# Kernel tuning notes

Hardware: AMD Instinct MI355X
Metric: run time of the kernel (lower is better)

## Reference

```python
import jax, jax.numpy as jnp
import numpy as np

B, S, H = 2, 2048, 1024
NH, HD = 16, 64
EPS = 1e-12
SCALE = float(np.sqrt(HD))


def layer_norm(x, g, b, eps=EPS):
    m = jnp.mean(x, axis=-1, keepdims=True)
    v = jnp.mean(jnp.square(x - m), axis=-1, keepdims=True)
    return (x - m) * jax.lax.rsqrt(v + eps) * g + b


def setup_inputs() -> dict:
    key = jax.random.key(0)
    ks = jax.random.split(key, 12)
    std = 0.02 / np.sqrt(2 * 24)  # num_hidden_layers = 24
    return {
        "hidden_states": jax.random.normal(ks[0], (B, S, H), dtype=jnp.float32),
        "attention_mask": jnp.ones((B, S), dtype=jnp.float32),
        "Wq": jax.random.normal(ks[1], (H, H), dtype=jnp.float32) * std,
        "bq": jnp.zeros((H,), dtype=jnp.float32),
        "Wk": jax.random.normal(ks[2], (H, H), dtype=jnp.float32) * std,
        "bk": jnp.zeros((H,), dtype=jnp.float32),
        "Wv": jax.random.normal(ks[3], (H, H), dtype=jnp.float32) * std,
        "bv": jnp.zeros((H,), dtype=jnp.float32),
        "Wd": jax.random.normal(ks[4], (H, H), dtype=jnp.float32) * (1.0 / np.sqrt(H)),
        "bd": jnp.zeros((H,), dtype=jnp.float32),
        "ln_g": jnp.ones((H,), dtype=jnp.float32),
        "ln_b": jnp.zeros((H,), dtype=jnp.float32),
    }


def reference(hidden_states, attention_mask, Wq, bq, Wk, bk, Wv, bv, Wd, bd, ln_g, ln_b):
    x = hidden_states
    # NOTE: source computes pre_attention_norm(x) but the no-cache path uses raw x for Q/K/V.
    def heads(t):  # [B,S,H] -> [B,NH,S,HD]
        return t.reshape(B, S, NH, HD).transpose(0, 2, 1, 3)

    q = heads(x @ Wq.T + bq)
    k = heads(x @ Wk.T + bk)
    v = heads(x @ Wv.T + bv)

    scores = jnp.einsum("bhqd,bhkd->bhqk", q, k) / SCALE
    mask = (1.0 - attention_mask) * -10000.0  # [B,S] -> broadcast [B,1,1,S]
    scores = scores + mask[:, None, None, :]
    probs = jax.nn.softmax(scores.astype(jnp.float32), axis=-1).astype(x.dtype)

    ctx = jnp.einsum("bhqk,bhkd->bhqd", probs, v)
    ctx = ctx.transpose(0, 2, 1, 3).reshape(B, S, NH * HD)

    out = ctx @ Wd.T + bd
    out = layer_norm(out + x, ln_g, ln_b)
    out = jnp.where(jnp.isfinite(out), out, jnp.zeros_like(out))
    return out
```

## Files before the change

### kernel.cpp

```cpp
#include <hip/hip_runtime.h>
#include <cstdint>
#include <cstddef>

#define B_    2
#define S_    2048
#define H_    1024
#define NH_   16
#define HD_   64

typedef __attribute__((ext_vector_type(8))) __bf16 bf16x8;
typedef __attribute__((ext_vector_type(4))) __bf16 bf16x4;
typedef __attribute__((ext_vector_type(4))) float  f32x4;
typedef __attribute__((ext_vector_type(2))) unsigned u32x2;

typedef __attribute__((address_space(1))) const unsigned int gcu32_t;
typedef __attribute__((address_space(3))) unsigned int lu32_t;
#define GLOAD16(gp, lp) __builtin_amdgcn_global_load_lds((gcu32_t*)(gp), (lu32_t*)(lp), 16, 0, 0)

#if __has_builtin(__builtin_amdgcn_exp2f)
#define EXP2F(x) __builtin_amdgcn_exp2f(x)
#else
#define EXP2F(x) exp2f(x)
#endif

#define SC_Q 0.1803368977f

__device__ __forceinline__ short f2bf(float f) {
  union { float f; unsigned u; } v; v.f = f;
  unsigned r = v.u + 0x7fffu + ((v.u >> 16) & 1u);
  return (short)(r >> 16);
}

__global__ __launch_bounds__(256) void convert_kernel(
    const float* __restrict__ x,  const float* __restrict__ wq,
    const float* __restrict__ wk, const float* __restrict__ wv,
    const float* __restrict__ wd,
    short* __restrict__ xb,  short* __restrict__ wqb, short* __restrict__ wkb,
    short* __restrict__ wvb, short* __restrict__ wdb) {
  size_t i = ((size_t)blockIdx.x * 256 + threadIdx.x) * 4;
  const float* src; short* dst; size_t off;
  if      (i < 4194304u) { src = x;  dst = xb;  off = i; }
  else if (i < 5242880u) { src = wq; dst = wqb; off = i - 4194304u; }
  else if (i < 6291456u) { src = wk; dst = wkb; off = i - 5242880u; }
  else if (i < 7340032u) { src = wv; dst = wvb; off = i - 6291456u; }
  else                   { src = wd; dst = wdb; off = i - 7340032u; }
  float4 v = *(const float4*)(src + off);
  short4 o; o.x = f2bf(v.x); o.y = f2bf(v.y); o.z = f2bf(v.z); o.w = f2bf(v.w);
  *(short4*)(dst + off) = o;
}

template<int MODE>
__global__ __launch_bounds__(256, 3) void gemm_bt(
    const short* __restrict__ A,
    const short* __restrict__ Bq, const short* __restrict__ Bk,
    const short* __restrict__ Bv,
    const float* __restrict__ biasq, const float* __restrict__ biask,
    const float* __restrict__ biasv,
    short* __restrict__ outq, short* __restrict__ outk, short* __restrict__ outv,
    float* __restrict__ outy) {
  __shared__ short As[128 * 64];
  __shared__ short Bs[128 * 64];

  const short* Bw; const float* bias; short* outs = nullptr;
  float qscale = 1.0f;
  if (MODE == 0) {
    int z = blockIdx.z;
    Bw   = (z == 0) ? Bq    : ((z == 1) ? Bk    : Bv);
    bias = (z == 0) ? biasq : ((z == 1) ? biask : biasv);
    outs = (z == 0) ? outq  : ((z == 1) ? outk  : outv);
    if (z == 0) qscale = SC_Q;
  } else {
    Bw = Bq; bias = biasq;
  }

  const int K = 1024;
  int tid  = threadIdx.x;
  int lane = tid & 63, w = tid >> 6;
  int wr = w >> 1, wc = w & 1;
  int m0 = blockIdx.y * 128, n0 = blockIdx.x * 128;
  int l15 = lane & 15, lg = lane >> 4;

  int lr = lane >> 3, lc8 = 8 * ((lane & 7) ^ lr);
  const short* Ag = A  + (size_t)(m0 + w * 8 + lr) * K + lc8;
  const short* Bg = Bw + (size_t)(n0 + w * 8 + lr) * K + lc8;

  int cxor = (l15 & 7) * 8;

  f32x4 acc[4][4];
  for (int m = 0; m < 4; m++)
    for (int n = 0; n < 4; n++) acc[m][n] = {0.f, 0.f, 0.f, 0.f};

  for (int kt = 0; kt < 16; kt++) {
    __syncthreads();
    for (int it = 0; it < 4; it++) {
      GLOAD16(Ag + (size_t)it * 32 * K + kt * 64, &As[(w * 8 + it * 32) * 64]);
      GLOAD16(Bg + (size_t)it * 32 * K + kt * 64, &Bs[(w * 8 + it * 32) * 64]);
    }
    __syncthreads();
    __builtin_amdgcn_s_setprio(1);
#pragma unroll
    for (int kkh = 0; kkh < 2; kkh++) {
      int col = (kkh * 32 + lg * 8) ^ cxor;
      bf16x8 af[4], bfr[4];
#pragma unroll
      for (int m = 0; m < 4; m++)
        af[m] = *(const bf16x8*)&As[(wr * 64 + m * 16 + l15) * 64 + col];
#pragma unroll
      for (int n = 0; n < 4; n++)
        bfr[n] = *(const bf16x8*)&Bs[(wc * 64 + n * 16 + l15) * 64 + col];
#pragma unroll
      for (int m = 0; m < 4; m++)
#pragma unroll
        for (int n = 0; n < 4; n++)
          acc[m][n] = __builtin_amdgcn_mfma_f32_16x16x32_bf16(af[m], bfr[n], acc[m][n], 0, 0, 0);
    }
    __builtin_amdgcn_s_setprio(0);
  }

  for (int n = 0; n < 4; n++) {
    int col = n0 + wc * 64 + n * 16 + l15;
    float bval = bias[col];
    if (MODE == 0) {
      int h = col >> 6, d = col & 63;
      for (int m = 0; m < 4; m++) {
        int rowb = m0 + wr * 64 + m * 16 + lg * 4;
        for (int j = 0; j < 4; j++) {
          int row = rowb + j;
          int bb = row >> 11, s = row & 2047;
          outs[(((size_t)bb * NH_ + h) * S_ + s) * HD_ + d] = f2bf((acc[m][n][j] + bval) * qscale);
        }
      }
    } else {
      for (int m = 0; m < 4; m++) {
        int rowb = m0 + wr * 64 + m * 16 + lg * 4;
        for (int j = 0; j < 4; j++)
          outy[(size_t)(rowb + j) * 1024 + col] = acc[m][n][j] + bval;
      }
    }
  }
}

__global__ __launch_bounds__(256, 2) void attn_kernel(
    const short* __restrict__ Q, const short* __restrict__ K,
    const short* __restrict__ V, const float* __restrict__ mask,
    short* __restrict__ ctx) {
  __shared__ short QPs[128 * 72];
  __shared__ short Ks[2][64 * 64];
  __shared__ short Vs[2][64 * 64];
  __shared__ float msk[2][64];

  int b = blockIdx.x;
  int bh = (b & 7) * 4 + ((b >> 3) >> 4);
  int qb = (b >> 3) & 15;
  int bidx = bh >> 4, h = bh & 15;
  int q0 = qb * 128;
  int tid = threadIdx.x, lane = tid & 63, w = tid >> 6;
  int l15 = lane & 15, lg = lane >> 4;

  const short* Qg = Q + (size_t)bh * S_ * HD_;
  const short* Kg = K + (size_t)bh * S_ * HD_;
  const short* Vg = V + (size_t)bh * S_ * HD_;

  int lr = lane >> 3, lc8 = 8 * ((lane & 7) ^ lr);
  int cxor = (l15 & 7) * 8;
  const float MLOG2E = -10000.0f * 1.442695041f;

  for (int it = 0; it < 4; it++) {
    int r = w * 8 + it * 32;
    GLOAD16(Qg + (size_t)(q0 + r + lr) * HD_ + lc8, &QPs[r * 64]);
  }
  for (int it = 0; it < 2; it++) {
    int r = w * 8 + it * 32;
    GLOAD16(Kg + (size_t)(r + lr) * HD_ + lc8, &Ks[0][r * 64]);
  }
  int vrow = tid >> 3, vcol = (tid & 7) * 8;
  int voff = ((vrow >> 2) * 4 + (vcol >> 4)) * 64 + (vrow & 3) * 16 + (vcol & 15);
  {
    int4 v0 = *(const int4*)&Vg[(size_t)vrow * HD_ + vcol];
    int4 v1 = *(const int4*)&Vg[(size_t)(vrow + 32) * HD_ + vcol];
    *(int4*)&Vs[0][voff] = v0;
    *(int4*)&Vs[0][voff + 2048] = v1;
  }
  if (tid < 64) msk[0][tid] = (1.0f - mask[bidx * S_ + tid]) * MLOG2E;
  __syncthreads();

  bf16x8 qreg[2][2];
#pragma unroll
  for (int kkh = 0; kkh < 2; kkh++)
#pragma unroll
    for (int qt = 0; qt < 2; qt++) {
      int row = w * 32 + qt * 16 + l15;
      qreg[kkh][qt] = *(const bf16x8*)&QPs[row * 64 + ((kkh * 32 + lg * 8) ^ cxor)];
    }
  __syncthreads();

  float mrun[2] = {-1e30f, -1e30f};
  float lrun[2] = {0.f, 0.f};
  f32x4 oacc[4][2];
#pragma unroll
  for (int dt = 0; dt < 4; dt++)
#pragma unroll
    for (int qt = 0; qt < 2; qt++) oacc[dt][qt] = {0.f, 0.f, 0.f, 0.f};

  unsigned vtrbase = (unsigned)(uintptr_t)&Vs[0][0] + (unsigned)(lg * 1024 + l15 * 8);
  int psrow = (w * 32 + l15) * 72;

  for (int kt = 0; kt < 32; kt++) {
    int cur = kt & 1;

    int4 vp0, vp1; float mp = 0.f;
    if (kt < 31) {
      const short* Kn = Kg + (size_t)(kt + 1) * 64 * HD_;
      for (int it = 0; it < 2; it++) {
        int r = w * 8 + it * 32;
        GLOAD16(Kn + (size_t)(r + lr) * HD_ + lc8, &Ks[cur ^ 1][r * 64]);
      }
      const short* Vn = Vg + (size_t)(kt + 1) * 64 * HD_;
      vp0 = *(const int4*)&Vn[(size_t)vrow * HD_ + vcol];
      vp1 = *(const int4*)&Vn[(size_t)(vrow + 32) * HD_ + vcol];
      if (tid < 64) mp = (1.0f - mask[bidx * S_ + (kt + 1) * 64 + tid]) * MLOG2E;
    }

    f32x4 sc[4][2];
#pragma unroll
    for (int n = 0; n < 4; n++)
#pragma unroll
      for (int qt = 0; qt < 2; qt++) sc[n][qt] = {0.f, 0.f, 0.f, 0.f};
    __builtin_amdgcn_s_setprio(1);
#pragma unroll
    for (int kkh = 0; kkh < 2; kkh++) {
      int col = (kkh * 32 + lg * 8) ^ cxor;
      bf16x8 kb[4];
#pragma unroll
      for (int n = 0; n < 4; n++)
        kb[n] = *(const bf16x8*)&Ks[cur][(n * 16 + l15) * 64 + col];
#pragma unroll
      for (int n = 0; n < 4; n++)
#pragma unroll
        for (int qt = 0; qt < 2; qt++)
          sc[n][qt] = __builtin_amdgcn_mfma_f32_16x16x32_bf16(kb[n], qreg[kkh][qt], sc[n][qt], 0, 0, 0);
    }
    __builtin_amdgcn_s_setprio(0);

    f32x4 mv[4];
#pragma unroll
    for (int n = 0; n < 4; n++)
      mv[n] = *(const f32x4*)&msk[cur][n * 16 + lg * 4];
    float rmax[2];
#pragma unroll
    for (int qt = 0; qt < 2; qt++) {
      float pm[4];
#pragma unroll
      for (int n = 0; n < 4; n++) {
        float t0 = sc[n][qt][0] + mv[n][0];
        float t1 = sc[n][qt][1] + mv[n][1];
        float t2 = sc[n][qt][2] + mv[n][2];
        float t3 = sc[n][qt][3] + mv[n][3];
        sc[n][qt][0] = t0; sc[n][qt][1] = t1; sc[n][qt][2] = t2; sc[n][qt][3] = t3;
        pm[n] = fmaxf(fmaxf(t0, t1), fmaxf(t2, t3));
      }
      float t = fmaxf(fmaxf(pm[0], pm[1]), fmaxf(pm[2], pm[3]));
      t = fmaxf(t, __shfl_xor(t, 16));
      t = fmaxf(t, __shfl_xor(t, 32));
      rmax[qt] = t;
    }

    int need = (rmax[0] > mrun[0] + 8.f) || (rmax[1] > mrun[1] + 8.f);
    if (__any(need)) {
#pragma unroll
      for (int qt = 0; qt < 2; qt++) {
        float mn = fmaxf(mrun[qt], rmax[qt]);
        float a = EXP2F(mrun[qt] - mn);
        lrun[qt] *= a;
        mrun[qt] = mn;
#pragma unroll
        for (int dt = 0; dt < 4; dt++)
#pragma unroll
          for (int j = 0; j < 4; j++) oacc[dt][qt][j] *= a;
      }
    }

    float rsum[2] = {0.f, 0.f};
#pragma unroll
    for (int n = 0; n < 4; n++)
#pragma unroll
      for (int qt = 0; qt < 2; qt++)
#pragma unroll
        for (int j = 0; j < 4; j++) {
          float p = EXP2F(sc[n][qt][j] - mrun[qt]);
          sc[n][qt][j] = p;
          rsum[qt] += p;
        }

#pragma unroll
    for (int qt = 0; qt < 2; qt++)
#pragma unroll
      for (int n = 0; n < 4; n++) {
        unsigned pk0, pk1;
        asm("v_cvt_pk_bf16_f32 %0, %1, %2" : "=v"(pk0) : "v"(sc[n][qt][0]), "v"(sc[n][qt][1]));
        asm("v_cvt_pk_bf16_f32 %0, %1, %2" : "=v"(pk1) : "v"(sc[n][qt][2]), "v"(sc[n][qt][3]));
        u32x2 wv2; wv2[0] = pk0; wv2[1] = pk1;
        *(u32x2*)&QPs[psrow + qt * 16 * 72 + n * 16 + lg * 4] = wv2;
      }

#pragma unroll
    for (int qt = 0; qt < 2; qt++) {
      float t = rsum[qt];
      t += __shfl_xor(t, 16);
      t += __shfl_xor(t, 32);
      lrun[qt] += t;
    }

    unsigned vtr = vtrbase + (unsigned)(cur * 8192);
#pragma unroll
    for (int kb = 0; kb < 2; kb++) {
      bf16x4 vlo[4], vhi[4];
#pragma unroll
      for (int dt = 0; dt < 4; dt++) {
        unsigned a = vtr + (unsigned)(kb * 4096 + dt * 128);
        asm volatile("ds_read_b64_tr_b16 %0, %2\n\t"
                     "ds_read_b64_tr_b16 %1, %2 offset:512"
                     : "=v"(vlo[dt]), "=v"(vhi[dt]) : "v"(a));
      }
      bf16x8 pb[2];
#pragma unroll
      for (int qt = 0; qt < 2; qt++)
        pb[qt] = *(const bf16x8*)&QPs[psrow + qt * 16 * 72 + kb * 32 + lg * 8];
      asm volatile("s_waitcnt lgkmcnt(0)" ::: "memory");
      __builtin_amdgcn_sched_barrier(0);
      __builtin_amdgcn_s_setprio(1);
#pragma unroll
      for (int dt = 0; dt < 4; dt++) {
        bf16x8 vb = __builtin_shufflevector(vlo[dt], vhi[dt], 0, 1, 2, 3, 4, 5, 6, 7);
#pragma unroll
        for (int qt = 0; qt < 2; qt++)
          oacc[dt][qt] = __builtin_amdgcn_mfma_f32_16x16x32_bf16(vb, pb[qt], oacc[dt][qt], 0, 0, 0);
      }
      __builtin_amdgcn_s_setprio(0);
    }

    if (kt < 31) {
      *(int4*)&Vs[cur ^ 1][voff] = vp0;
      *(int4*)&Vs[cur ^ 1][voff + 2048] = vp1;
      if (tid < 64) msk[cur ^ 1][tid] = mp;
    }
    __syncthreads();
  }

#pragma unroll
  for (int qt = 0; qt < 2; qt++) {
    float inv = 1.0f / lrun[qt];
    int sg = q0 + w * 32 + qt * 16 + l15;
    size_t rowbase = ((size_t)(bidx * S_ + sg)) * H_ + h * HD_;
#pragma unroll
    for (int dt = 0; dt < 4; dt++) {
      short4 st;
      st.x = f2bf(oacc[dt][qt][0] * inv);
      st.y = f2bf(oacc[dt][qt][1] * inv);
      st.z = f2bf(oacc[dt][qt][2] * inv);
      st.w = f2bf(oacc[dt][qt][3] * inv);
      *(short4*)&ctx[rowbase + dt * 16 + lg * 4] = st;
    }
  }
}

__global__ __launch_bounds__(256) void ln_kernel(
    const float* __restrict__ y, const float* __restrict__ x,
    const float* __restrict__ g, const float* __restrict__ bta,
    float* __restrict__ out) {
  __shared__ float red[4];
  int row = blockIdx.x;
  int tid = threadIdx.x, lane = tid & 63, w = tid >> 6;
  size_t base = (size_t)row * 1024 + tid * 4;
  float4 yv = *(const float4*)(y + base);
  float4 xv = *(const float4*)(x + base);
  float v0 = yv.x + xv.x, v1 = yv.y + xv.y, v2 = yv.z + xv.z, v3 = yv.w + xv.w;

  float ssum = v0 + v1 + v2 + v3;
  for (int off = 1; off < 64; off <<= 1) ssum += __shfl_xor(ssum, off);
  if (lane == 0) red[w] = ssum;
  __syncthreads();
  float mean = (red[0] + red[1] + red[2] + red[3]) * (1.f / 1024.f);
  __syncthreads();

  float d0 = v0 - mean, d1 = v1 - mean, d2 = v2 - mean, d3 = v3 - mean;
  float sq = d0 * d0 + d1 * d1 + d2 * d2 + d3 * d3;
  for (int off = 1; off < 64; off <<= 1) sq += __shfl_xor(sq, off);
  if (lane == 0) red[w] = sq;
  __syncthreads();
  float var = (red[0] + red[1] + red[2] + red[3]) * (1.f / 1024.f);
  float rs = 1.0f / sqrtf(var + 1e-12f);

  int c = tid * 4;
  float4 gv = *(const float4*)(g + c);
  float4 bv = *(const float4*)(bta + c);
  float o0 = d0 * rs * gv.x + bv.x;
  float o1 = d1 * rs * gv.y + bv.y;
  float o2 = d2 * rs * gv.z + bv.z;
  float o3 = d3 * rs * gv.w + bv.w;
  float4 ov;
  ov.x = __builtin_isfinite(o0) ? o0 : 0.f;
  ov.y = __builtin_isfinite(o1) ? o1 : 0.f;
  ov.z = __builtin_isfinite(o2) ? o2 : 0.f;
  ov.w = __builtin_isfinite(o3) ? o3 : 0.f;
  *(float4*)(out + base) = ov;
}

extern "C" void kernel_launch(void* const* d_in, const int* in_sizes, int n_in,
                              void* d_out, int out_size, void* d_ws, size_t ws_size,
                              hipStream_t stream) {
  (void)in_sizes; (void)n_in; (void)out_size; (void)ws_size;
  const float* x    = (const float*)d_in[0];
  const float* mask = (const float*)d_in[1];
  const float* Wq   = (const float*)d_in[2];
  const float* bq   = (const float*)d_in[3];
  const float* Wk   = (const float*)d_in[4];
  const float* bk   = (const float*)d_in[5];
  const float* Wv   = (const float*)d_in[6];
  const float* bv   = (const float*)d_in[7];
  const float* Wd   = (const float*)d_in[8];
  const float* bd   = (const float*)d_in[9];
  const float* ln_g = (const float*)d_in[10];
  const float* ln_b = (const float*)d_in[11];
  float* out = (float*)d_out;

  char* ws = (char*)d_ws;
  short* xb   = (short*)(ws);
  short* wqb  = (short*)(ws + ( 8ull << 20));
  short* wkb  = (short*)(ws + (10ull << 20));
  short* wvb  = (short*)(ws + (12ull << 20));
  short* wdb  = (short*)(ws + (14ull << 20));
  short* qb   = (short*)(ws + (16ull << 20));
  short* kb   = (short*)(ws + (24ull << 20));
  short* vb   = (short*)(ws + (32ull << 20));
  short* ctxb = (short*)(ws + (40ull << 20));
  float* y    = (float*)(ws + (48ull << 20));

  convert_kernel<<<8192, 256, 0, stream>>>(x, Wq, Wk, Wv, Wd, xb, wqb, wkb, wvb, wdb);
  gemm_bt<0><<<dim3(8, 32, 3), 256, 0, stream>>>(xb, wqb, wkb, wvb, bq, bk, bv,
                                                 qb, kb, vb, nullptr);
  attn_kernel<<<512, 256, 0, stream>>>(qb, kb, vb, mask, ctxb);
  gemm_bt<1><<<dim3(8, 32, 1), 256, 0, stream>>>(ctxb, wdb, nullptr, nullptr, bd,
                                                 nullptr, nullptr, nullptr, nullptr,
                                                 nullptr, y);
  ln_kernel<<<4096, 256, 0, stream>>>(y, x, ln_g, ln_b, out);
}
```

Baseline: 222.3 us.

## Split attention block into 8 waves with 16 query rows each

The attention kernel goes from 4 waves handling 32 query rows each to 8 waves of 16 rows each (512 threads per block). Each thread now does one K/V tile load chunk and carries half the accumulators. This cuts per-wave register pressure and gives more waves to hide latency, but each K tile fragment read from LDS is reused by only one query tile instead of two. It also drops the s_setprio hints from the GEMM inner loop.

```diff
diff --git a/kernel.cpp b/kernel.cpp
--- a/kernel.cpp
+++ b/kernel.cpp
@@ -97,7 +97,6 @@
       GLOAD16(Bg + (size_t)it * 32 * K + kt * 64, &Bs[(w * 8 + it * 32) * 64]);
     }
     __syncthreads();
-    __builtin_amdgcn_s_setprio(1);
 #pragma unroll
     for (int kkh = 0; kkh < 2; kkh++) {
       int col = (kkh * 32 + lg * 8) ^ cxor;
@@ -114,7 +113,6 @@
         for (int n = 0; n < 4; n++)
           acc[m][n] = __builtin_amdgcn_mfma_f32_16x16x32_bf16(af[m], bfr[n], acc[m][n], 0, 0, 0);
     }
-    __builtin_amdgcn_s_setprio(0);
   }
 
   for (int n = 0; n < 4; n++) {
@@ -140,7 +138,7 @@
   }
 }
 
-__global__ __launch_bounds__(256, 2) void attn_kernel(
+__global__ __launch_bounds__(512, 4) void attn_kernel(
     const short* __restrict__ Q, const short* __restrict__ K,
     const short* __restrict__ V, const float* __restrict__ mask,
     short* __restrict__ ctx) {
@@ -165,202 +163,153 @@
   int cxor = (l15 & 7) * 8;
   const float MLOG2E = -10000.0f * 1.442695041f;
 
-  for (int it = 0; it < 4; it++) {
-    int r = w * 8 + it * 32;
+#pragma unroll
+  for (int it = 0; it < 2; it++) {
+    int r = w * 8 + it * 64;
     GLOAD16(Qg + (size_t)(q0 + r + lr) * HD_ + lc8, &QPs[r * 64]);
   }
-  for (int it = 0; it < 2; it++) {
-    int r = w * 8 + it * 32;
-    GLOAD16(Kg + (size_t)(r + lr) * HD_ + lc8, &Ks[0][r * 64]);
-  }
+  GLOAD16(Kg + (size_t)(w * 8 + lr) * HD_ + lc8, &Ks[0][(w * 8) * 64]);
   int vrow = tid >> 3, vcol = (tid & 7) * 8;
   int voff = ((vrow >> 2) * 4 + (vcol >> 4)) * 64 + (vrow & 3) * 16 + (vcol & 15);
-  {
-    int4 v0 = *(const int4*)&Vg[(size_t)vrow * HD_ + vcol];
-    int4 v1 = *(const int4*)&Vg[(size_t)(vrow + 32) * HD_ + vcol];
-    *(int4*)&Vs[0][voff] = v0;
-    *(int4*)&Vs[0][voff + 2048] = v1;
-  }
+  *(int4*)&Vs[0][voff] = *(const int4*)&Vg[(size_t)vrow * HD_ + vcol];
   if (tid < 64) msk[0][tid] = (1.0f - mask[bidx * S_ + tid]) * MLOG2E;
   __syncthreads();
 
-  bf16x8 qreg[2][2];
-#pragma unroll
-  for (int kkh = 0; kkh < 2; kkh++)
-#pragma unroll
-    for (int qt = 0; qt < 2; qt++) {
-      int row = w * 32 + qt * 16 + l15;
-      qreg[kkh][qt] = *(const bf16x8*)&QPs[row * 64 + ((kkh * 32 + lg * 8) ^ cxor)];
-    }
-  __syncthreads();
-
-  float mrun[2] = {-1e30f, -1e30f};
-  float lrun[2] = {0.f, 0.f};
-  f32x4 oacc[4][2];
-#pragma unroll
-  for (int dt = 0; dt < 4; dt++)
-#pragma unroll
-    for (int qt = 0; qt < 2; qt++) oacc[dt][qt] = {0.f, 0.f, 0.f, 0.f};
+  bf16x8 qreg[2];
+#pragma unroll
+  for (int kkh = 0; kkh < 2; kkh++) {
+    int row = w * 16 + l15;
+    qreg[kkh] = *(const bf16x8*)&QPs[row * 64 + ((kkh * 32 + lg * 8) ^ cxor)];
+  }
+  __syncthreads();
+
+  float mrun = -1e30f, lrun = 0.f;
+  f32x4 oacc[4];
+#pragma unroll
+  for (int dt = 0; dt < 4; dt++) oacc[dt] = {0.f, 0.f, 0.f, 0.f};
 
   unsigned vtrbase = (unsigned)(uintptr_t)&Vs[0][0] + (unsigned)(lg * 1024 + l15 * 8);
-  int psrow = (w * 32 + l15) * 72;
+  int psrow = (w * 16 + l15) * 72;
 
   for (int kt = 0; kt < 32; kt++) {
     int cur = kt & 1;
 
-    int4 vp0, vp1; float mp = 0.f;
+    int4 vp0; float mp = 0.f;
     if (kt < 31) {
       const short* Kn = Kg + (size_t)(kt + 1) * 64 * HD_;
-      for (int it = 0; it < 2; it++) {
-        int r = w * 8 + it * 32;
-        GLOAD16(Kn + (size_t)(r + lr) * HD_ + lc8, &Ks[cur ^ 1][r * 64]);
-      }
+      GLOAD16(Kn + (size_t)(w * 8 + lr) * HD_ + lc8, &Ks[cur ^ 1][(w * 8) * 64]);
       const short* Vn = Vg + (size_t)(kt + 1) * 64 * HD_;
       vp0 = *(const int4*)&Vn[(size_t)vrow * HD_ + vcol];
-      vp1 = *(const int4*)&Vn[(size_t)(vrow + 32) * HD_ + vcol];
       if (tid < 64) mp = (1.0f - mask[bidx * S_ + (kt + 1) * 64 + tid]) * MLOG2E;
     }
 
-    f32x4 sc[4][2];
-#pragma unroll
-    for (int n = 0; n < 4; n++)
-#pragma unroll
-      for (int qt = 0; qt < 2; qt++) sc[n][qt] = {0.f, 0.f, 0.f, 0.f};
+    f32x4 sc[4];
+#pragma unroll
+    for (int n = 0; n < 4; n++) sc[n] = {0.f, 0.f, 0.f, 0.f};
     __builtin_amdgcn_s_setprio(1);
 #pragma unroll
     for (int kkh = 0; kkh < 2; kkh++) {
       int col = (kkh * 32 + lg * 8) ^ cxor;
-      bf16x8 kb[4];
+      bf16x8 kbf[4];
 #pragma unroll
       for (int n = 0; n < 4; n++)
-        kb[n] = *(const bf16x8*)&Ks[cur][(n * 16 + l15) * 64 + col];
+        kbf[n] = *(const bf16x8*)&Ks[cur][(n * 16 + l15) * 64 + col];
 #pragma unroll
       for (int n = 0; n < 4; n++)
-#pragma unroll
-        for (int qt = 0; qt < 2; qt++)
-          sc[n][qt] = __builtin_amdgcn_mfma_f32_16x16x32_bf16(kb[n], qreg[kkh][qt], sc[n][qt], 0, 0, 0);
+        sc[n] = __builtin_amdgcn_mfma_f32_16x16x32_bf16(kbf[n], qreg[kkh], sc[n], 0, 0, 0);
     }
     __builtin_amdgcn_s_setprio(0);
 
-    f32x4 mv[4];
+    float pm[4];
+#pragma unroll
+    for (int n = 0; n < 4; n++) {
+      f32x4 mv = *(const f32x4*)&msk[cur][n * 16 + lg * 4];
+      float t0 = sc[n][0] + mv[0];
+      float t1 = sc[n][1] + mv[1];
+      float t2 = sc[n][2] + mv[2];
+      float t3 = sc[n][3] + mv[3];
+      sc[n][0] = t0; sc[n][1] = t1; sc[n][2] = t2; sc[n][3] = t3;
+      pm[n] = fmaxf(fmaxf(t0, t1), fmaxf(t2, t3));
+    }
+    float rmax = fmaxf(fmaxf(pm[0], pm[1]), fmaxf(pm[2], pm[3]));
+    rmax = fmaxf(rmax, __shfl_xor(rmax, 16));
+    rmax = fmaxf(rmax, __shfl_xor(rmax, 32));
+
+    if (__any(rmax > mrun + 8.f)) {
+      float mn = fmaxf(mrun, rmax);
+      float a = EXP2F(mrun - mn);
+      lrun *= a;
+      mrun = mn;
+#pragma unroll
+      for (int dt = 0; dt < 4; dt++)
+#pragma unroll
+        for (int j = 0; j < 4; j++) oacc[dt][j] *= a;
+    }
+
+    float rs_ = 0.f;
 #pragma unroll
     for (int n = 0; n < 4; n++)
-      mv[n] = *(const f32x4*)&msk[cur][n * 16 + lg * 4];
-    float rmax[2];
-#pragma unroll
-    for (int qt = 0; qt < 2; qt++) {
-      float pm[4];
-#pragma unroll
-      for (int n = 0; n < 4; n++) {
-        float t0 = sc[n][qt][0] + mv[n][0];
-        float t1 = sc[n][qt][1] + mv[n][1];
-        float t2 = sc[n][qt][2] + mv[n][2];
-        float t3 = sc[n][qt][3] + mv[n][3];
-        sc[n][qt][0] = t0; sc[n][qt][1] = t1; sc[n][qt][2] = t2; sc[n][qt][3] = t3;
-        pm[n] = fmaxf(fmaxf(t0, t1), fmaxf(t2, t3));
-      }
-      float t = fmaxf(fmaxf(pm[0], pm[1]), fmaxf(pm[2], pm[3]));
-      t = fmaxf(t, __shfl_xor(t, 16));
-      t = fmaxf(t, __shfl_xor(t, 32));
-      rmax[qt] = t;
-    }
-
-    int need = (rmax[0] > mrun[0] + 8.f) || (rmax[1] > mrun[1] + 8.f);
-    if (__any(need)) {
-#pragma unroll
-      for (int qt = 0; qt < 2; qt++) {
-        float mn = fmaxf(mrun[qt], rmax[qt]);
-        float a = EXP2F(mrun[qt] - mn);
-        lrun[qt] *= a;
-        mrun[qt] = mn;
-#pragma unroll
-        for (int dt = 0; dt < 4; dt++)
-#pragma unroll
-          for (int j = 0; j < 4; j++) oacc[dt][qt][j] *= a;
-      }
-    }
-
-    float rsum[2] = {0.f, 0.f};
-#pragma unroll
-    for (int n = 0; n < 4; n++)
-#pragma unroll
-      for (int qt = 0; qt < 2; qt++)
-#pragma unroll
-        for (int j = 0; j < 4; j++) {
-          float p = EXP2F(sc[n][qt][j] - mrun[qt]);
-          sc[n][qt][j] = p;
-          rsum[qt] += p;
-        }
-
-#pragma unroll
-    for (int qt = 0; qt < 2; qt++)
-#pragma unroll
-      for (int n = 0; n < 4; n++) {
-        unsigned pk0, pk1;
-        asm("v_cvt_pk_bf16_f32 %0, %1, %2" : "=v"(pk0) : "v"(sc[n][qt][0]), "v"(sc[n][qt][1]));
-        asm("v_cvt_pk_bf16_f32 %0, %1, %2" : "=v"(pk1) : "v"(sc[n][qt][2]), "v"(sc[n][qt][3]));
-        u32x2 wv2; wv2[0] = pk0; wv2[1] = pk1;
-        *(u32x2*)&QPs[psrow + qt * 16 * 72 + n * 16 + lg * 4] = wv2;
-      }
-
-#pragma unroll
-    for (int qt = 0; qt < 2; qt++) {
-      float t = rsum[qt];
-      t += __shfl_xor(t, 16);
-      t += __shfl_xor(t, 32);
-      lrun[qt] += t;
-    }
+#pragma unroll
+      for (int j = 0; j < 4; j++) {
+        float p = EXP2F(sc[n][j] - mrun);
+        sc[n][j] = p;
+        rs_ += p;
+      }
+
+#pragma unroll
+    for (int n = 0; n < 4; n++) {
+      unsigned pk0, pk1;
+      asm("v_cvt_pk_bf16_f32 %0, %1, %2" : "=v"(pk0) : "v"(sc[n][0]), "v"(sc[n][1]));
+      asm("v_cvt_pk_bf16_f32 %0, %1, %2" : "=v"(pk1) : "v"(sc[n][2]), "v"(sc[n][3]));
+      u32x2 wv2; wv2[0] = pk0; wv2[1] = pk1;
+      *(u32x2*)&QPs[psrow + n * 16 + lg * 4] = wv2;
+    }
+
+    rs_ += __shfl_xor(rs_, 16);
+    rs_ += __shfl_xor(rs_, 32);
+    lrun += rs_;
 
     unsigned vtr = vtrbase + (unsigned)(cur * 8192);
 #pragma unroll
-    for (int kb = 0; kb < 2; kb++) {
+    for (int kb2 = 0; kb2 < 2; kb2++) {
       bf16x4 vlo[4], vhi[4];
 #pragma unroll
       for (int dt = 0; dt < 4; dt++) {
-        unsigned a = vtr + (unsigned)(kb * 4096 + dt * 128);
+        unsigned a = vtr + (unsigned)(kb2 * 4096 + dt * 128);
         asm volatile("ds_read_b64_tr_b16 %0, %2\n\t"
                      "ds_read_b64_tr_b16 %1, %2 offset:512"
                      : "=v"(vlo[dt]), "=v"(vhi[dt]) : "v"(a));
       }
-      bf16x8 pb[2];
-#pragma unroll
-      for (int qt = 0; qt < 2; qt++)
-        pb[qt] = *(const bf16x8*)&QPs[psrow + qt * 16 * 72 + kb * 32 + lg * 8];
+      bf16x8 pb = *(const bf16x8*)&QPs[psrow + kb2 * 32 + lg * 8];
       asm volatile("s_waitcnt lgkmcnt(0)" ::: "memory");
       __builtin_amdgcn_sched_barrier(0);
       __builtin_amdgcn_s_setprio(1);
 #pragma unroll
       for (int dt = 0; dt < 4; dt++) {
         bf16x8 vb = __builtin_shufflevector(vlo[dt], vhi[dt], 0, 1, 2, 3, 4, 5, 6, 7);
-#pragma unroll
-        for (int qt = 0; qt < 2; qt++)
-          oacc[dt][qt] = __builtin_amdgcn_mfma_f32_16x16x32_bf16(vb, pb[qt], oacc[dt][qt], 0, 0, 0);
+        oacc[dt] = __builtin_amdgcn_mfma_f32_16x16x32_bf16(vb, pb, oacc[dt], 0, 0, 0);
       }
       __builtin_amdgcn_s_setprio(0);
     }
 
     if (kt < 31) {
       *(int4*)&Vs[cur ^ 1][voff] = vp0;
-      *(int4*)&Vs[cur ^ 1][voff + 2048] = vp1;
       if (tid < 64) msk[cur ^ 1][tid] = mp;
     }
     __syncthreads();
   }
 
-#pragma unroll
-  for (int qt = 0; qt < 2; qt++) {
-    float inv = 1.0f / lrun[qt];
-    int sg = q0 + w * 32 + qt * 16 + l15;
-    size_t rowbase = ((size_t)(bidx * S_ + sg)) * H_ + h * HD_;
-#pragma unroll
-    for (int dt = 0; dt < 4; dt++) {
-      short4 st;
-      st.x = f2bf(oacc[dt][qt][0] * inv);
-      st.y = f2bf(oacc[dt][qt][1] * inv);
-      st.z = f2bf(oacc[dt][qt][2] * inv);
-      st.w = f2bf(oacc[dt][qt][3] * inv);
-      *(short4*)&ctx[rowbase + dt * 16 + lg * 4] = st;
-    }
+  float inv = 1.0f / lrun;
+  int sg = q0 + w * 16 + l15;
+  size_t rowbase = ((size_t)(bidx * S_ + sg)) * H_ + h * HD_;
+#pragma unroll
+  for (int dt = 0; dt < 4; dt++) {
+    short4 st;
+    st.x = f2bf(oacc[dt][0] * inv);
+    st.y = f2bf(oacc[dt][1] * inv);
+    st.z = f2bf(oacc[dt][2] * inv);
+    st.w = f2bf(oacc[dt][3] * inv);
+    *(short4*)&ctx[rowbase + dt * 16 + lg * 4] = st;
   }
 }
 
@@ -439,7 +388,7 @@
   convert_kernel<<<8192, 256, 0, stream>>>(x, Wq, Wk, Wv, Wd, xb, wqb, wkb, wvb, wdb);
   gemm_bt<0><<<dim3(8, 32, 3), 256, 0, stream>>>(xb, wqb, wkb, wvb, bq, bk, bv,
                                                  qb, kb, vb, nullptr);
-  attn_kernel<<<512, 256, 0, stream>>>(qb, kb, vb, mask, ctxb);
+  attn_kernel<<<512, 512, 0, stream>>>(qb, kb, vb, mask, ctxb);
   gemm_bt<1><<<dim3(8, 32, 1), 256, 0, stream>>>(ctxb, wdb, nullptr, nullptr, bd,
                                                  nullptr, nullptr, nullptr, nullptr,
                                                  nullptr, y);
```

After: 226.6 us. No clear change (+1.9%).
